# Kernel optimization log

Hardware: AMD Instinct MI355X
Metric: run time of the kernel (lower is better)

The kernel has to match this reference:

```python
import jax, jax.numpy as jnp
import numpy as np

HEAD_DIM = 64

def setup_inputs() -> dict:
    key = jax.random.key(0)
    k1, k2, k3, k4, k5 = jax.random.split(key, 5)
    T, B, E = 2048, 4, 1024
    KD = 64  # kdim
    x = jax.random.normal(k1, (T, B, E), dtype=jnp.float32)
    in_proj_weight = jax.random.normal(k2, (3 * KD, HEAD_DIM), dtype=jnp.float32) * (1.0 / np.sqrt(HEAD_DIM))
    in_proj_bias = jnp.zeros((3 * KD,), dtype=jnp.float32)
    out_w = jax.random.normal(k4, (HEAD_DIM, KD), dtype=jnp.float32) * (1.0 / np.sqrt(KD))
    out_b = jnp.zeros((HEAD_DIM,), dtype=jnp.float32)
    return {"x": x, "in_proj_weight": in_proj_weight, "in_proj_bias": in_proj_bias,
            "out_w": out_w, "out_b": out_b}

def reference(x, in_proj_weight, in_proj_bias, out_w, out_b):
    # x: [T, B, E] with E = H * HEAD_DIM (qkv_same self-attention path)
    T, B, E = x.shape
    H = E // HEAD_DIM
    KD = in_proj_weight.shape[0] // 3
    scaling = HEAD_DIM ** (-0.5)
    # reshape splits embed dim into heads: [T, B*H, 64]
    xh = x.reshape(T, B * H, HEAD_DIM)
    # fused in-projection: [T, B*H, 3*KD], then chunk into q/k/v
    qkv = xh @ in_proj_weight.T + in_proj_bias
    q, k, v = jnp.split(qkv, 3, axis=-1)          # each [T, B*H, KD]
    q = q * scaling
    q = q.transpose(1, 0, 2)                      # [B*H, T, KD]
    k = k.transpose(1, 0, 2)
    v = v.transpose(1, 0, 2)
    scores = jnp.einsum('btd,bsd->bts', q, k)     # [B*H, T, T]
    w = jax.nn.softmax(scores, axis=-1)
    attn = jnp.einsum('bts,bsd->btd', w, v)       # [B*H, T, KD]
    attn = attn.transpose(1, 0, 2).reshape(T, B, H, KD)
    out = attn @ out_w.T + out_b                  # [T, B, H, HEAD_DIM]
    out = out.reshape(T, B, H * HEAD_DIM)         # [T, B, E]
    # averaged attention weights over heads: [B, T, T]
    avg_w = w.reshape(B, H, T, T).sum(axis=1) / H
    return out, avg_w
```

## Files before the change

### kernel.cpp

```cpp
#include <hip/hip_runtime.h>
#include <hip/hip_bf16.h>

#define T_DIM 2048
#define B_DIM 4
#define E_DIM 1024

typedef __bf16 bf16_t;
typedef bf16_t bf16x8 __attribute__((ext_vector_type(8)));
typedef float f32x4 __attribute__((ext_vector_type(4)));
typedef float f32x16 __attribute__((ext_vector_type(16)));

union frag_u { uint4 u; bf16x8 b; };

constexpr float SCALEQ = 0.18033688011112042f;

__device__ __forceinline__ f32x16 mfma32(bf16x8 a, bf16x8 b, f32x16 c) {
  return __builtin_amdgcn_mfma_f32_32x32x16_bf16(a, b, c, 0, 0, 0);
}
__device__ __forceinline__ unsigned packbf(float a, float b) {
  union { bf16_t h[2]; unsigned u; } r;
  r.h[0] = (bf16_t)a; r.h[1] = (bf16_t)b; return r.u;
}
__device__ __forceinline__ void pl32swap(unsigned &x, unsigned &y) {
  asm volatile("v_permlane32_swap_b32 %0, %1" : "+v"(x), "+v"(y));
}
__device__ __forceinline__ void gload16(const void* g, void* l) {
  __builtin_amdgcn_global_load_lds((const __attribute__((address_space(1))) void*)g,
                                   (__attribute__((address_space(3))) void*)l, 16, 0, 0);
}
__device__ __forceinline__ bf16x8 ldc(const char* base, int chunk, int row) {
  frag_u f; f.u = *(const uint4*)(base + chunk * 1024 + row * 16); return f.b;
}
__device__ __forceinline__ float ex2(float x) { return __builtin_amdgcn_exp2f(x); }

#define VMCNT4 do { asm volatile("s_waitcnt vmcnt(4)" ::: "memory"); \
                    __builtin_amdgcn_sched_barrier(0); } while (0)
#define VMCNT0 do { asm volatile("s_waitcnt vmcnt(0)" ::: "memory"); \
                    __builtin_amdgcn_sched_barrier(0); } while (0)
#define LGKM0  do { asm volatile("s_waitcnt lgkmcnt(0)" ::: "memory"); \
                    __builtin_amdgcn_sched_barrier(0); } while (0)
#define SBAR   do { __builtin_amdgcn_s_barrier(); \
                    __builtin_amdgcn_sched_barrier(0); } while (0)

template <int O>
__device__ __forceinline__ uint4 mkfrag(const f32x16& A) {
  unsigned X = packbf(A[O + 0], A[O + 1]);
  unsigned Z = packbf(A[O + 2], A[O + 3]);
  unsigned Y = packbf(A[O + 4], A[O + 5]);
  unsigned W = packbf(A[O + 6], A[O + 7]);
  pl32swap(X, Y); pl32swap(Z, W);
  return (uint4){X, Z, Y, W};
}

__global__ __launch_bounds__(256) void qkv_kernel(
    const float* __restrict__ x, const float* __restrict__ W,
    const float* __restrict__ bias,
    bf16_t* __restrict__ Qc, bf16_t* __restrict__ Kc, bf16_t* __restrict__ Vc) {
  __shared__ __align__(16) char xlds[16384];
  __shared__ __align__(16) char wlds[24576];
  __shared__ float bs[192];
  const int tid = threadIdx.x;
  const int bh = blockIdx.x >> 4;
  const int tt = blockIdx.x & 15;
  const int b = bh >> 4, h = bh & 15;
  const int t0 = tt * 128;
  const int wid = tid >> 6, lane = tid & 63;
  const int lq = lane & 31, hi = lane >> 5;

  for (int i = tid; i < 1024; i += 256) {
    int t = i >> 3, oct = i & 7;
    const float* src = x + ((size_t)(t0 + t) * B_DIM + b) * E_DIM + h * 64 + oct * 8;
    float4 f0 = *(const float4*)src;
    float4 f1 = *(const float4*)(src + 4);
    uint4 u;
    u.x = packbf(f0.x, f0.y); u.y = packbf(f0.z, f0.w);
    u.z = packbf(f1.x, f1.y); u.w = packbf(f1.z, f1.w);
    *(uint4*)(xlds + oct * 2048 + t * 16) = u;
  }
  for (int i = tid; i < 1536; i += 256) {
    int r = i >> 3, oct = i & 7;
    const float* src = W + r * 64 + oct * 8;
    float4 f0 = *(const float4*)src;
    float4 f1 = *(const float4*)(src + 4);
    uint4 u;
    u.x = packbf(f0.x, f0.y); u.y = packbf(f0.z, f0.w);
    u.z = packbf(f1.x, f1.y); u.w = packbf(f1.z, f1.w);
    *(uint4*)(wlds + oct * 3072 + r * 16) = u;
  }
  if (tid < 192) bs[tid] = bias[tid];
  __syncthreads();

  frag_u bx[4];
  #pragma unroll
  for (int s = 0; s < 4; ++s)
    bx[s].u = *(const uint4*)(xlds + (s * 2 + hi) * 2048 + (wid * 32 + lq) * 16);

  f32x16 acc[6];
  #pragma unroll
  for (int mt = 0; mt < 6; ++mt)
    #pragma unroll
    for (int r = 0; r < 16; ++r) acc[mt][r] = 0.f;

  #pragma unroll
  for (int mt = 0; mt < 6; ++mt) {
    #pragma unroll
    for (int s = 0; s < 4; ++s) {
      frag_u aw;
      aw.u = *(const uint4*)(wlds + (s * 2 + hi) * 3072 + (mt * 32 + lq) * 16);
      acc[mt] = mfma32(aw.b, bx[s].b, acc[mt]);
    }
  }

  const size_t tb = ((size_t)bh * 32 + (t0 >> 6) + (wid >> 1)) * 4096;
  const int trow = (wid & 1) * 32 + lq;

  #pragma unroll
  for (int mt = 0; mt < 6; ++mt) {
    #pragma unroll
    for (int g = 0; g < 4; ++g) {
      int rbase = mt * 32 + 8 * g + 4 * hi;
      float4 bq = *(const float4*)&bs[rbase];
      float v0 = acc[mt][4 * g + 0] + bq.x;
      float v1 = acc[mt][4 * g + 1] + bq.y;
      float v2 = acc[mt][4 * g + 2] + bq.z;
      float v3 = acc[mt][4 * g + 3] + bq.w;
      if (mt < 2) {
        union { ushort4 us; unsigned u2[2]; } pk;
        pk.u2[0] = packbf(v0 * SCALEQ, v1 * SCALEQ);
        pk.u2[1] = packbf(v2 * SCALEQ, v3 * SCALEQ);
        int d0 = rbase;
        *(ushort4*)(Qc + tb + (d0 >> 3) * 512 + trow * 8 + (d0 & 7)) = pk.us;
      } else if (mt < 4) {
        union { ushort4 us; unsigned u2[2]; } pk;
        pk.u2[0] = packbf(v0, v1);
        pk.u2[1] = packbf(v2, v3);
        int d0 = rbase - 64;
        *(ushort4*)(Kc + tb + (d0 >> 3) * 512 + trow * 8 + (d0 & 7)) = pk.us;
      } else {
        int d0 = rbase - 128;
        bf16_t* vdst = Vc + tb + (trow >> 3) * 512 + (trow & 7);
        vdst[(size_t)(d0 + 0) * 8] = (bf16_t)v0;
        vdst[(size_t)(d0 + 1) * 8] = (bf16_t)v1;
        vdst[(size_t)(d0 + 2) * 8] = (bf16_t)v2;
        vdst[(size_t)(d0 + 3) * 8] = (bf16_t)v3;
      }
    }
  }
}

__global__ __launch_bounds__(256, 2) void flash_kernel(
    const bf16_t* __restrict__ Qc, const bf16_t* __restrict__ Kc,
    const bf16_t* __restrict__ Vc,
    const float* __restrict__ Wo, const float* __restrict__ bo,
    float* __restrict__ out, float* __restrict__ Lv) {
  __shared__ __align__(16) char lds[32768];
  __shared__ __align__(16) char wlds[8192];
  const int tid = threadIdx.x;
  const int bid = ((blockIdx.x & 7) << 6) | (blockIdx.x >> 3);
  const int bh = bid >> 3, qb = bid & 7;
  const int b = bh >> 4, h = bh & 15;
  const int wid = tid >> 6, lane = tid & 63;
  const int lq = lane & 31, hi = lane >> 5;
  const int qw = qb * 256 + wid * 64;

  for (int i = tid; i < 512; i += 256) {
    int d = i >> 3, oct = i & 7;
    const float* src = Wo + d * 64 + oct * 8;
    float4 f0 = *(const float4*)src;
    float4 f1 = *(const float4*)(src + 4);
    uint4 u;
    u.x = packbf(f0.x, f0.y); u.y = packbf(f0.z, f0.w);
    u.z = packbf(f1.x, f1.y); u.w = packbf(f1.z, f1.w);
    *(uint4*)(wlds + oct * 1024 + d * 16) = u;
  }

  const bf16_t* qtb = Qc + ((size_t)bh * 32 + (qw >> 6)) * 4096;
  frag_u qfA[4], qfB[4];
  #pragma unroll
  for (int s = 0; s < 4; ++s) {
    qfA[s].u = *(const uint4*)(qtb + (s * 2 + hi) * 512 + lq * 8);
    qfB[s].u = *(const uint4*)(qtb + (s * 2 + hi) * 512 + (32 + lq) * 8);
  }

  frag_u ones;
  #pragma unroll
  for (int j = 0; j < 8; ++j) ones.b[j] = (bf16_t)1.0f;

  f32x16 zc;
  #pragma unroll
  for (int i = 0; i < 16; ++i) zc[i] = 0.f;

  f32x16 oA0, oA1, oB0, oB1, lmfA, lmfB;
  #pragma unroll
  for (int i = 0; i < 16; ++i) {
    oA0[i] = 0.f; oA1[i] = 0.f; oB0[i] = 0.f; oB1[i] = 0.f;
    lmfA[i] = 0.f; lmfB[i] = 0.f;
  }

  const bf16_t* kbh = Kc + (size_t)bh * 131072;
  const bf16_t* vbh = Vc + (size_t)bh * 131072;
  auto stage = [&](int buf, int t) {
    char* kl_ = lds + buf * 16384 + wid * 1024;
    char* vl_ = kl_ + 8192;
    const bf16_t* kt = kbh + (size_t)t * 4096 + wid * 512 + lane * 8;
    const bf16_t* vt = vbh + (size_t)t * 4096 + wid * 512 + lane * 8;
    gload16(kt, kl_); gload16(kt + 2048, kl_ + 4096);
    gload16(vt, vl_); gload16(vt + 2048, vl_ + 4096);
  };

  stage(0, 0); stage(1, 1);
  VMCNT4; LGKM0;
  SBAR;

  for (int t = 0; t < 32; ++t) {
    const char* kl = lds + (t & 1) * 16384;
    const char* vl = kl + 8192;

    bf16x8 k0[4], k1[4];
    #pragma unroll
    for (int s = 0; s < 4; ++s) {
      k0[s] = ldc(kl, s * 2 + hi, lq);
      k1[s] = ldc(kl, s * 2 + hi, 32 + lq);
    }
    f32x16 aA0, aA1, aB0, aB1;
    __builtin_amdgcn_s_setprio(1);
    aA0 = mfma32(k0[0], qfA[0].b, zc);
    aA1 = mfma32(k1[0], qfA[0].b, zc);
    aB0 = mfma32(k0[0], qfB[0].b, zc);
    aB1 = mfma32(k1[0], qfB[0].b, zc);
    #pragma unroll
    for (int s = 1; s < 4; ++s) {
      aA0 = mfma32(k0[s], qfA[s].b, aA0);
      aA1 = mfma32(k1[s], qfA[s].b, aA1);
      aB0 = mfma32(k0[s], qfB[s].b, aB0);
      aB1 = mfma32(k1[s], qfB[s].b, aB1);
    }
    __builtin_amdgcn_s_setprio(0);

    bf16x8 v0[4], v1[4];
    #pragma unroll
    for (int ks = 0; ks < 4; ++ks) {
      v0[ks] = ldc(vl, ks * 2 + hi, lq);
      v1[ks] = ldc(vl, ks * 2 + hi, 32 + lq);
    }
    LGKM0;
    SBAR;
    if (t + 2 < 32) stage(t & 1, t + 2);

    #pragma unroll
    for (int i = 0; i < 16; ++i) {
      aA0[i] = ex2(aA0[i]); aA1[i] = ex2(aA1[i]);
      aB0[i] = ex2(aB0[i]); aB1[i] = ex2(aB1[i]);
    }

    frag_u pA0, pA1, pA2, pA3, pB0, pB1, pB2, pB3;
    pA0.u = mkfrag<0>(aA0); pA1.u = mkfrag<8>(aA0);
    pA2.u = mkfrag<0>(aA1); pA3.u = mkfrag<8>(aA1);
    pB0.u = mkfrag<0>(aB0); pB1.u = mkfrag<8>(aB0);
    pB2.u = mkfrag<0>(aB1); pB3.u = mkfrag<8>(aB1);

    __builtin_amdgcn_s_setprio(1);
    oA0 = mfma32(v0[0], pA0.b, oA0); oA1 = mfma32(v1[0], pA0.b, oA1);
    oB0 = mfma32(v0[0], pB0.b, oB0); oB1 = mfma32(v1[0], pB0.b, oB1);
    oA0 = mfma32(v0[1], pA1.b, oA0); oA1 = mfma32(v1[1], pA1.b, oA1);
    oB0 = mfma32(v0[1], pB1.b, oB0); oB1 = mfma32(v1[1], pB1.b, oB1);
    oA0 = mfma32(v0[2], pA2.b, oA0); oA1 = mfma32(v1[2], pA2.b, oA1);
    oB0 = mfma32(v0[2], pB2.b, oB0); oB1 = mfma32(v1[2], pB2.b, oB1);
    oA0 = mfma32(v0[3], pA3.b, oA0); oA1 = mfma32(v1[3], pA3.b, oA1);
    oB0 = mfma32(v0[3], pB3.b, oB0); oB1 = mfma32(v1[3], pB3.b, oB1);
    lmfA = mfma32(ones.b, pA0.b, lmfA); lmfA = mfma32(ones.b, pA1.b, lmfA);
    lmfA = mfma32(ones.b, pA2.b, lmfA); lmfA = mfma32(ones.b, pA3.b, lmfA);
    lmfB = mfma32(ones.b, pB0.b, lmfB); lmfB = mfma32(ones.b, pB1.b, lmfB);
    lmfB = mfma32(ones.b, pB2.b, lmfB); lmfB = mfma32(ones.b, pB3.b, lmfB);
    __builtin_amdgcn_s_setprio(0);

    if (t < 30) { VMCNT4; } else { VMCNT0; }
    SBAR;
  }

  float ltA = lmfA[0], ltB = lmfB[0];
  float iA = 1.f / ltA, iB = 1.f / ltB;
  #pragma unroll
  for (int i = 0; i < 16; ++i) { oA0[i] *= iA; oA1[i] *= iA; oB0[i] *= iB; oB1[i] *= iB; }

  frag_u fA[4], fB[4];
  fA[0].u = mkfrag<0>(oA0); fA[1].u = mkfrag<8>(oA0);
  fA[2].u = mkfrag<0>(oA1); fA[3].u = mkfrag<8>(oA1);
  fB[0].u = mkfrag<0>(oB0); fB[1].u = mkfrag<8>(oB0);
  fB[2].u = mkfrag<0>(oB1); fB[3].u = mkfrag<8>(oB1);

  f32x16 cA0, cA1, cB0, cB1;
  #pragma unroll
  for (int i = 0; i < 16; ++i) { cA0[i] = 0.f; cA1[i] = 0.f; cB0[i] = 0.f; cB1[i] = 0.f; }
  #pragma unroll
  for (int s = 0; s < 4; ++s) {
    frag_u w0, w1;
    w0.u = *(const uint4*)(wlds + (s * 2 + hi) * 1024 + lq * 16);
    w1.u = *(const uint4*)(wlds + (s * 2 + hi) * 1024 + (32 + lq) * 16);
    cA0 = mfma32(fA[s].b, w0.b, cA0);
    cA1 = mfma32(fA[s].b, w1.b, cA1);
    cB0 = mfma32(fB[s].b, w0.b, cB0);
    cB1 = mfma32(fB[s].b, w1.b, cB1);
  }
  float bo0 = bo[lq], bo1 = bo[32 + lq];
  #pragma unroll
  for (int r = 0; r < 16; ++r) {
    int trA = qw + (r & 3) + 8 * (r >> 2) + 4 * hi;
    int trB = trA + 32;
    out[((size_t)trA * B_DIM + b) * E_DIM + h * 64 + lq]      = cA0[r] + bo0;
    out[((size_t)trA * B_DIM + b) * E_DIM + h * 64 + 32 + lq] = cA1[r] + bo1;
    out[((size_t)trB * B_DIM + b) * E_DIM + h * 64 + lq]      = cB0[r] + bo0;
    out[((size_t)trB * B_DIM + b) * E_DIM + h * 64 + 32 + lq] = cB1[r] + bo1;
  }
  if (lane < 32) {
    Lv[(size_t)bh * T_DIM + qw + lq] = ltA;
    Lv[(size_t)bh * T_DIM + qw + 32 + lq] = ltB;
  }
}

__global__ __launch_bounds__(512, 2) void avgw_kernel(
    const bf16_t* __restrict__ Qc, const bf16_t* __restrict__ Kc,
    const float* __restrict__ Lv, float* __restrict__ avgw) {
  __shared__ __align__(16) char qlds[2][16384];
  __shared__ __align__(16) char klds[2][16384];
  __shared__ float lw[16][128];
  const int tid = threadIdx.x;
  const int bid = ((blockIdx.x & 7) << 7) | (blockIdx.x >> 3);
  const int b = bid >> 8, tq = (bid >> 4) & 15, sq = bid & 15;
  const int t0 = tq * 128, s0 = sq * 128;
  const int wid = tid >> 6, lane = tid & 63;
  const int lq = lane & 31, hi = lane >> 5;
  const int wr = wid >> 2, wc = wid & 3;

  for (int i = tid; i < 2048; i += 512) {
    int h = i >> 7, tt = i & 127;
    size_t idx = ((size_t)(b * 16 + h)) * T_DIM + t0 + tt;
    lw[h][tt] = 1.0f / (16.0f * Lv[idx]);
  }

  auto stage = [&](int buf, int h) {
    int bh = b * 16 + h;
    const bf16_t* qt = Qc + ((size_t)bh * 32 + (t0 >> 6)) * 4096;
    const bf16_t* kt = Kc + ((size_t)bh * 32 + (s0 >> 6)) * 4096;
    #pragma unroll
    for (int j = 0; j < 2; ++j) {
      gload16(qt + wid * 1024 + j * 512 + lane * 8, qlds[buf] + wid * 2048 + j * 1024);
      gload16(kt + wid * 1024 + j * 512 + lane * 8, klds[buf] + wid * 2048 + j * 1024);
    }
  };

  f32x16 zc;
  #pragma unroll
  for (int r = 0; r < 16; ++r) zc[r] = 0.f;

  f32x16 sacc[2];
  #pragma unroll
  for (int i = 0; i < 2; ++i)
    #pragma unroll
    for (int r = 0; r < 16; ++r) sacc[i][r] = 0.f;

  stage(0, 0);
  __syncthreads();

  for (int h = 0; h < 16; ++h) {
    if (h < 15) stage((h + 1) & 1, h + 1);
    const char* qb = qlds[h & 1];
    const char* kb = klds[h & 1];

    frag_u aq[2][4], ak[4];
    #pragma unroll
    for (int s = 0; s < 4; ++s) {
      int rk = wc * 32 + lq;
      ak[s].u = *(const uint4*)(kb + (rk >> 6) * 8192 + (s * 2 + hi) * 1024 + (rk & 63) * 16);
      #pragma unroll
      for (int i = 0; i < 2; ++i) {
        int rq = wr * 64 + i * 32 + lq;
        aq[i][s].u = *(const uint4*)(qb + (rq >> 6) * 8192 + (s * 2 + hi) * 1024 + (rq & 63) * 16);
      }
    }

    #pragma unroll
    for (int i = 0; i < 2; ++i) {
      __builtin_amdgcn_s_setprio(1);
      f32x16 c = mfma32(aq[i][0].b, ak[0].b, zc);
      #pragma unroll
      for (int s = 1; s < 4; ++s) c = mfma32(aq[i][s].b, ak[s].b, c);
      __builtin_amdgcn_s_setprio(0);
      #pragma unroll
      for (int g = 0; g < 4; ++g) {
        f32x4 l4 = *(const f32x4*)&lw[h][wr * 64 + i * 32 + 8 * g + 4 * hi];
        #pragma unroll
        for (int e = 0; e < 4; ++e)
          sacc[i][4 * g + e] += ex2(c[4 * g + e]) * l4[e];
      }
    }
    __syncthreads();
  }

  #pragma unroll
  for (int i = 0; i < 2; ++i)
    #pragma unroll
    for (int r = 0; r < 16; ++r) {
      int trow = t0 + wr * 64 + i * 32 + (r & 3) + ((r >> 2) << 3) + (hi << 2);
      int scol = s0 + wc * 32 + lq;
      avgw[((size_t)b * T_DIM + trow) * T_DIM + scol] = sacc[i][r];
    }
}

extern "C" void kernel_launch(void* const* d_in, const int* in_sizes, int n_in,
                              void* d_out, int out_size, void* d_ws, size_t ws_size,
                              hipStream_t stream) {
  const float* x    = (const float*)d_in[0];
  const float* W    = (const float*)d_in[1];
  const float* bias = (const float*)d_in[2];
  const float* Wo   = (const float*)d_in[3];
  const float* bo   = (const float*)d_in[4];
  float* out  = (float*)d_out;
  float* avgw = out + (size_t)T_DIM * B_DIM * E_DIM;

  char* ws = (char*)d_ws;
  bf16_t* Qc = (bf16_t*)(ws);
  bf16_t* Kc = (bf16_t*)(ws + (16u << 20));
  bf16_t* Vc = (bf16_t*)(ws + (32u << 20));
  float*  Lv = (float*)(ws + (48u << 20));

  qkv_kernel<<<dim3(1024), dim3(256), 0, stream>>>(x, W, bias, Qc, Kc, Vc);
  flash_kernel<<<dim3(512), dim3(256), 0, stream>>>(Qc, Kc, Vc, Wo, bo, out, Lv);
  avgw_kernel<<<dim3(1024), dim3(512), 0, stream>>>(Qc, Kc, Lv, avgw);
}
```

Baseline: 168.6 us.

## Replace LDS-staged async loads with direct global fragment loads in flash and avgw

Removes the double-buffered global_load_lds staging of K/V tiles in the flash kernel and of Q/K tiles in the avgw kernel. Each wave now loads its MFMA fragments straight from global memory (through the caches), which also drops the per-iteration barriers and waitcnt syncs. The Wo tile is now read and converted to bf16 per wave instead of being shared through LDS, and the flash block-index swizzle is simplified. This frees LDS and cuts barrier stalls, at the cost of redundant global or L2 traffic across waves and no explicit prefetch overlap.

```diff
diff --git a/kernel.cpp b/kernel.cpp
--- a/kernel.cpp
+++ b/kernel.cpp
@@ -24,23 +24,7 @@
 __device__ __forceinline__ void pl32swap(unsigned &x, unsigned &y) {
   asm volatile("v_permlane32_swap_b32 %0, %1" : "+v"(x), "+v"(y));
 }
-__device__ __forceinline__ void gload16(const void* g, void* l) {
-  __builtin_amdgcn_global_load_lds((const __attribute__((address_space(1))) void*)g,
-                                   (__attribute__((address_space(3))) void*)l, 16, 0, 0);
-}
-__device__ __forceinline__ bf16x8 ldc(const char* base, int chunk, int row) {
-  frag_u f; f.u = *(const uint4*)(base + chunk * 1024 + row * 16); return f.b;
-}
 __device__ __forceinline__ float ex2(float x) { return __builtin_amdgcn_exp2f(x); }
-
-#define VMCNT4 do { asm volatile("s_waitcnt vmcnt(4)" ::: "memory"); \
-                    __builtin_amdgcn_sched_barrier(0); } while (0)
-#define VMCNT0 do { asm volatile("s_waitcnt vmcnt(0)" ::: "memory"); \
-                    __builtin_amdgcn_sched_barrier(0); } while (0)
-#define LGKM0  do { asm volatile("s_waitcnt lgkmcnt(0)" ::: "memory"); \
-                    __builtin_amdgcn_sched_barrier(0); } while (0)
-#define SBAR   do { __builtin_amdgcn_s_barrier(); \
-                    __builtin_amdgcn_sched_barrier(0); } while (0)
 
 template <int O>
 __device__ __forceinline__ uint4 mkfrag(const f32x16& A) {
@@ -153,27 +137,14 @@
     const bf16_t* __restrict__ Vc,
     const float* __restrict__ Wo, const float* __restrict__ bo,
     float* __restrict__ out, float* __restrict__ Lv) {
-  __shared__ __align__(16) char lds[32768];
-  __shared__ __align__(16) char wlds[8192];
   const int tid = threadIdx.x;
-  const int bid = ((blockIdx.x & 7) << 6) | (blockIdx.x >> 3);
-  const int bh = bid >> 3, qb = bid & 7;
+  const int bh = blockIdx.x & 63;
+  const int qb = blockIdx.x >> 6;
   const int b = bh >> 4, h = bh & 15;
   const int wid = tid >> 6, lane = tid & 63;
   const int lq = lane & 31, hi = lane >> 5;
   const int qw = qb * 256 + wid * 64;
 
-  for (int i = tid; i < 512; i += 256) {
-    int d = i >> 3, oct = i & 7;
-    const float* src = Wo + d * 64 + oct * 8;
-    float4 f0 = *(const float4*)src;
-    float4 f1 = *(const float4*)(src + 4);
-    uint4 u;
-    u.x = packbf(f0.x, f0.y); u.y = packbf(f0.z, f0.w);
-    u.z = packbf(f1.x, f1.y); u.w = packbf(f1.z, f1.w);
-    *(uint4*)(wlds + oct * 1024 + d * 16) = u;
-  }
-
   const bf16_t* qtb = Qc + ((size_t)bh * 32 + (qw >> 6)) * 4096;
   frag_u qfA[4], qfB[4];
   #pragma unroll
@@ -199,29 +170,22 @@
 
   const bf16_t* kbh = Kc + (size_t)bh * 131072;
   const bf16_t* vbh = Vc + (size_t)bh * 131072;
-  auto stage = [&](int buf, int t) {
-    char* kl_ = lds + buf * 16384 + wid * 1024;
-    char* vl_ = kl_ + 8192;
-    const bf16_t* kt = kbh + (size_t)t * 4096 + wid * 512 + lane * 8;
-    const bf16_t* vt = vbh + (size_t)t * 4096 + wid * 512 + lane * 8;
-    gload16(kt, kl_); gload16(kt + 2048, kl_ + 4096);
-    gload16(vt, vl_); gload16(vt + 2048, vl_ + 4096);
-  };
-
-  stage(0, 0); stage(1, 1);
-  VMCNT4; LGKM0;
-  SBAR;
 
   for (int t = 0; t < 32; ++t) {
-    const char* kl = lds + (t & 1) * 16384;
-    const char* vl = kl + 8192;
-
-    bf16x8 k0[4], k1[4];
+    const bf16_t* kt = kbh + (size_t)t * 4096;
+    const bf16_t* vt = vbh + (size_t)t * 4096;
+
+    bf16x8 k0[4], k1[4], v0[4], v1[4];
     #pragma unroll
     for (int s = 0; s < 4; ++s) {
-      k0[s] = ldc(kl, s * 2 + hi, lq);
-      k1[s] = ldc(kl, s * 2 + hi, 32 + lq);
-    }
+      frag_u f0, f1, g0, g1;
+      f0.u = *(const uint4*)(kt + (s * 2 + hi) * 512 + lq * 8);
+      f1.u = *(const uint4*)(kt + (s * 2 + hi) * 512 + (32 + lq) * 8);
+      g0.u = *(const uint4*)(vt + (s * 2 + hi) * 512 + lq * 8);
+      g1.u = *(const uint4*)(vt + (s * 2 + hi) * 512 + (32 + lq) * 8);
+      k0[s] = f0.b; k1[s] = f1.b; v0[s] = g0.b; v1[s] = g1.b;
+    }
+
     f32x16 aA0, aA1, aB0, aB1;
     __builtin_amdgcn_s_setprio(1);
     aA0 = mfma32(k0[0], qfA[0].b, zc);
@@ -236,16 +200,6 @@
       aB1 = mfma32(k1[s], qfB[s].b, aB1);
     }
     __builtin_amdgcn_s_setprio(0);
-
-    bf16x8 v0[4], v1[4];
-    #pragma unroll
-    for (int ks = 0; ks < 4; ++ks) {
-      v0[ks] = ldc(vl, ks * 2 + hi, lq);
-      v1[ks] = ldc(vl, ks * 2 + hi, 32 + lq);
-    }
-    LGKM0;
-    SBAR;
-    if (t + 2 < 32) stage(t & 1, t + 2);
 
     #pragma unroll
     for (int i = 0; i < 16; ++i) {
@@ -273,9 +227,6 @@
     lmfB = mfma32(ones.b, pB0.b, lmfB); lmfB = mfma32(ones.b, pB1.b, lmfB);
     lmfB = mfma32(ones.b, pB2.b, lmfB); lmfB = mfma32(ones.b, pB3.b, lmfB);
     __builtin_amdgcn_s_setprio(0);
-
-    if (t < 30) { VMCNT4; } else { VMCNT0; }
-    SBAR;
   }
 
   float ltA = lmfA[0], ltB = lmfB[0];
@@ -295,8 +246,18 @@
   #pragma unroll
   for (int s = 0; s < 4; ++s) {
     frag_u w0, w1;
-    w0.u = *(const uint4*)(wlds + (s * 2 + hi) * 1024 + lq * 16);
-    w1.u = *(const uint4*)(wlds + (s * 2 + hi) * 1024 + (32 + lq) * 16);
+    {
+      const float* ws0 = Wo + lq * 64 + (s * 2 + hi) * 8;
+      float4 a = *(const float4*)ws0;
+      float4 c = *(const float4*)(ws0 + 4);
+      w0.u = (uint4){packbf(a.x, a.y), packbf(a.z, a.w),
+                     packbf(c.x, c.y), packbf(c.z, c.w)};
+      const float* ws1 = Wo + (32 + lq) * 64 + (s * 2 + hi) * 8;
+      float4 d = *(const float4*)ws1;
+      float4 e = *(const float4*)(ws1 + 4);
+      w1.u = (uint4){packbf(d.x, d.y), packbf(d.z, d.w),
+                     packbf(e.x, e.y), packbf(e.z, e.w)};
+    }
     cA0 = mfma32(fA[s].b, w0.b, cA0);
     cA1 = mfma32(fA[s].b, w1.b, cA1);
     cB0 = mfma32(fB[s].b, w0.b, cB0);
@@ -321,8 +282,6 @@
 __global__ __launch_bounds__(512, 2) void avgw_kernel(
     const bf16_t* __restrict__ Qc, const bf16_t* __restrict__ Kc,
     const float* __restrict__ Lv, float* __restrict__ avgw) {
-  __shared__ __align__(16) char qlds[2][16384];
-  __shared__ __align__(16) char klds[2][16384];
   __shared__ float lw[16][128];
   const int tid = threadIdx.x;
   const int bid = ((blockIdx.x & 7) << 7) | (blockIdx.x >> 3);
@@ -337,17 +296,7 @@
     size_t idx = ((size_t)(b * 16 + h)) * T_DIM + t0 + tt;
     lw[h][tt] = 1.0f / (16.0f * Lv[idx]);
   }
-
-  auto stage = [&](int buf, int h) {
-    int bh = b * 16 + h;
-    const bf16_t* qt = Qc + ((size_t)bh * 32 + (t0 >> 6)) * 4096;
-    const bf16_t* kt = Kc + ((size_t)bh * 32 + (s0 >> 6)) * 4096;
-    #pragma unroll
-    for (int j = 0; j < 2; ++j) {
-      gload16(qt + wid * 1024 + j * 512 + lane * 8, qlds[buf] + wid * 2048 + j * 1024);
-      gload16(kt + wid * 1024 + j * 512 + lane * 8, klds[buf] + wid * 2048 + j * 1024);
-    }
-  };
+  __syncthreads();
 
   f32x16 zc;
   #pragma unroll
@@ -359,24 +308,19 @@
     #pragma unroll
     for (int r = 0; r < 16; ++r) sacc[i][r] = 0.f;
 
-  stage(0, 0);
-  __syncthreads();
+  const int krow = (wc & 1) * 32 + lq;
 
   for (int h = 0; h < 16; ++h) {
-    if (h < 15) stage((h + 1) & 1, h + 1);
-    const char* qb = qlds[h & 1];
-    const char* kb = klds[h & 1];
+    const int bh = b * 16 + h;
+    const bf16_t* qh = Qc + ((size_t)bh * 32 + (t0 >> 6) + wr) * 4096;
+    const bf16_t* kh = Kc + ((size_t)bh * 32 + (s0 >> 6) + (wc >> 1)) * 4096;
 
     frag_u aq[2][4], ak[4];
     #pragma unroll
     for (int s = 0; s < 4; ++s) {
-      int rk = wc * 32 + lq;
-      ak[s].u = *(const uint4*)(kb + (rk >> 6) * 8192 + (s * 2 + hi) * 1024 + (rk & 63) * 16);
-      #pragma unroll
-      for (int i = 0; i < 2; ++i) {
-        int rq = wr * 64 + i * 32 + lq;
-        aq[i][s].u = *(const uint4*)(qb + (rq >> 6) * 8192 + (s * 2 + hi) * 1024 + (rq & 63) * 16);
-      }
+      ak[s].u = *(const uint4*)(kh + (s * 2 + hi) * 512 + krow * 8);
+      aq[0][s].u = *(const uint4*)(qh + (s * 2 + hi) * 512 + lq * 8);
+      aq[1][s].u = *(const uint4*)(qh + (s * 2 + hi) * 512 + (32 + lq) * 8);
     }
 
     #pragma unroll
@@ -394,7 +338,6 @@
           sacc[i][4 * g + e] += ex2(c[4 * g + e]) * l4[e];
       }
     }
-    __syncthreads();
   }
 
   #pragma unroll
```

New measurement: 181.7 us. +7.8%, slower.

## Replace MFMA row-sum with scalar accumulation and simplify avgw block mapping

Applied to the files above, without the earlier changes.

The softmax denominator is no longer computed with eight extra MFMAs against a ones fragment per tile. Each lane now sums its exponentiated scores in fp32 registers, and the two half-waves are combined with a lane shuffle at the end. This frees matrix-core issue slots and two 16-float accumulators, at the cost of extra VALU adds in the exp loop. Separately, the avgw kernel's XCD-swizzled block index is replaced by a direct mapping, which changes which blocks share L2 on each XCD. The lane-local sum is in fp32 rather than summing the bf16-rounded probabilities, so the normalizer differs slightly.

```diff
diff --git a/kernel.cpp b/kernel.cpp
--- a/kernel.cpp
+++ b/kernel.cpp
@@ -182,20 +182,14 @@
     qfB[s].u = *(const uint4*)(qtb + (s * 2 + hi) * 512 + (32 + lq) * 8);
   }
 
-  frag_u ones;
-  #pragma unroll
-  for (int j = 0; j < 8; ++j) ones.b[j] = (bf16_t)1.0f;
-
   f32x16 zc;
   #pragma unroll
   for (int i = 0; i < 16; ++i) zc[i] = 0.f;
 
-  f32x16 oA0, oA1, oB0, oB1, lmfA, lmfB;
-  #pragma unroll
-  for (int i = 0; i < 16; ++i) {
-    oA0[i] = 0.f; oA1[i] = 0.f; oB0[i] = 0.f; oB1[i] = 0.f;
-    lmfA[i] = 0.f; lmfB[i] = 0.f;
-  }
+  f32x16 oA0, oA1, oB0, oB1;
+  #pragma unroll
+  for (int i = 0; i < 16; ++i) { oA0[i] = 0.f; oA1[i] = 0.f; oB0[i] = 0.f; oB1[i] = 0.f; }
+  float lAacc = 0.f, lBacc = 0.f;
 
   const bf16_t* kbh = Kc + (size_t)bh * 131072;
   const bf16_t* vbh = Vc + (size_t)bh * 131072;
@@ -247,11 +241,15 @@
     SBAR;
     if (t + 2 < 32) stage(t & 1, t + 2);
 
+    float sA = 0.f, sB = 0.f;
     #pragma unroll
     for (int i = 0; i < 16; ++i) {
-      aA0[i] = ex2(aA0[i]); aA1[i] = ex2(aA1[i]);
-      aB0[i] = ex2(aB0[i]); aB1[i] = ex2(aB1[i]);
-    }
+      aA0[i] = ex2(aA0[i]); sA += aA0[i];
+      aA1[i] = ex2(aA1[i]); sA += aA1[i];
+      aB0[i] = ex2(aB0[i]); sB += aB0[i];
+      aB1[i] = ex2(aB1[i]); sB += aB1[i];
+    }
+    lAacc += sA; lBacc += sB;
 
     frag_u pA0, pA1, pA2, pA3, pB0, pB1, pB2, pB3;
     pA0.u = mkfrag<0>(aA0); pA1.u = mkfrag<8>(aA0);
@@ -268,17 +266,14 @@
     oB0 = mfma32(v0[2], pB2.b, oB0); oB1 = mfma32(v1[2], pB2.b, oB1);
     oA0 = mfma32(v0[3], pA3.b, oA0); oA1 = mfma32(v1[3], pA3.b, oA1);
     oB0 = mfma32(v0[3], pB3.b, oB0); oB1 = mfma32(v1[3], pB3.b, oB1);
-    lmfA = mfma32(ones.b, pA0.b, lmfA); lmfA = mfma32(ones.b, pA1.b, lmfA);
-    lmfA = mfma32(ones.b, pA2.b, lmfA); lmfA = mfma32(ones.b, pA3.b, lmfA);
-    lmfB = mfma32(ones.b, pB0.b, lmfB); lmfB = mfma32(ones.b, pB1.b, lmfB);
-    lmfB = mfma32(ones.b, pB2.b, lmfB); lmfB = mfma32(ones.b, pB3.b, lmfB);
     __builtin_amdgcn_s_setprio(0);
 
     if (t < 30) { VMCNT4; } else { VMCNT0; }
     SBAR;
   }
 
-  float ltA = lmfA[0], ltB = lmfB[0];
+  float ltA = lAacc + __shfl_xor(lAacc, 32);
+  float ltB = lBacc + __shfl_xor(lBacc, 32);
   float iA = 1.f / ltA, iB = 1.f / ltB;
   #pragma unroll
   for (int i = 0; i < 16; ++i) { oA0[i] *= iA; oA1[i] *= iA; oB0[i] *= iB; oB1[i] *= iB; }
@@ -325,8 +320,10 @@
   __shared__ __align__(16) char klds[2][16384];
   __shared__ float lw[16][128];
   const int tid = threadIdx.x;
-  const int bid = ((blockIdx.x & 7) << 7) | (blockIdx.x >> 3);
-  const int b = bid >> 8, tq = (bid >> 4) & 15, sq = bid & 15;
+  const int n = blockIdx.x;
+  const int sq = (n & 7) | (((n >> 3) & 1) << 3);
+  const int tq = (n >> 4) & 15;
+  const int b = n >> 8;
   const int t0 = tq * 128, s0 = sq * 128;
   const int wid = tid >> 6, lane = tid & 63;
   const int lq = lane & 31, hi = lane >> 5;
```

Measured after the change: 174.8 us. +3.7%, slower.
